# Optimization experiments

Measured on AMD Instinct MI355X. Metric: run time of the kernel, lower is better.

## Reference

```python
import jax, jax.numpy as jnp
import numpy as np

MESSAGE_SIZE = 128
MESSAGE_PASSES = 3
N_BONDS = 7      # Single, Double, Triple, Quadruple, Aromatic, Pi, Universal
N_LAYERS = 8     # 8 bias-free Linear layers, ReLU after the first 7
N_TYPES = 6      # top-4 ranked atoms + atom 0, plus catchall slot (index 5)
ATOM_VALS = [6.0, 7.0, 8.0, 9.0, 16.0, 17.0, 1.0]
TOP_ATOMS = [6.0, 7.0, 8.0, 9.0, 0.0]


def setup_inputs() -> dict:
    key = jax.random.key(0)
    ks = jax.random.split(key, 8)
    B, N, F, D = 128, 128, 75, MESSAGE_SIZE
    g = jax.random.uniform(ks[0], (B, N_BONDS, N, N), dtype=jnp.float32)
    h = jax.random.normal(ks[1], (B, N, F), dtype=jnp.float32)
    # channel 0 carries the atomic number used for GRU routing
    atom_ids = jax.random.randint(ks[2], (B, N), 0, len(ATOM_VALS))
    h = h.at[:, :, 0].set(jnp.asarray(ATOM_VALS, jnp.float32)[atom_ids])
    s = 1.0 / np.sqrt(D)
    msg_W = jax.random.normal(ks[3], (N_BONDS, N_LAYERS, D, D), jnp.float32) * s
    gru_Wih = jax.random.normal(ks[4], (2, N_TYPES, 3 * D, D), jnp.float32) * s  # [regular/universal, type, 3H, H]
    gru_Whh = jax.random.normal(ks[5], (2, N_TYPES, 3 * D, D), jnp.float32) * s
    gru_bih = jax.random.normal(ks[6], (2, N_TYPES, 3 * D), jnp.float32) * s
    gru_bhh = jax.random.normal(ks[7], (2, N_TYPES, 3 * D), jnp.float32) * s
    return dict(g=g, h=h, msg_W=msg_W, gru_Wih=gru_Wih, gru_Whh=gru_Whh,
                gru_bih=gru_bih, gru_bhh=gru_bhh)


def _gru_grouped(x, hx, tid, Wih, Whh, bih, bhh):
    """torch.nn.GRUCell(input=x, hx=hx) with per-node parameter group tid in [0,T).
    Wih/Whh: [T, 3H, H], bih/bhh: [T, 3H]."""
    gx = jnp.einsum('nd,tgd->ntg', x, Wih)   # [n, T, 3H]
    gh = jnp.einsum('nd,tgd->ntg', hx, Whh)
    gx = jnp.take_along_axis(gx, tid[:, None, None], axis=1)[:, 0] + bih[tid]
    gh = jnp.take_along_axis(gh, tid[:, None, None], axis=1)[:, 0] + bhh[tid]
    xr, xz, xn = jnp.split(gx, 3, axis=-1)
    hr, hz, hn = jnp.split(gh, 3, axis=-1)
    r = jax.nn.sigmoid(xr + hr)
    z = jax.nn.sigmoid(xz + hz)
    n = jnp.tanh(xn + r * hn)
    return (1.0 - z) * n + z * hx


def reference(g, h, msg_W, gru_Wih, gru_Whh, gru_bih, gru_bhh):
    B, N, F = h.shape
    D = msg_W.shape[-1]
    h_t = jnp.concatenate([h, jnp.zeros((B, N, D - F), h.dtype)], axis=2)  # [B,N,D]
    atoms = h[:, :, 0].reshape(-1)
    tid = jnp.full(atoms.shape, N_TYPES - 1, jnp.int32)  # default catchall
    for i, a in enumerate(TOP_ATOMS):
        tid = jnp.where(atoms == jnp.float32(a), jnp.int32(i), tid)
    for _ in range(MESSAGE_PASSES):
        # per-bond-type 8-layer bias-free MLP, vectorized over the 7 bond types
        xb = jnp.broadcast_to(h_t[None], (N_BONDS, B, N, D))
        for l in range(N_LAYERS):
            xb = jnp.einsum('kbnd,ked->kbne', xb, msg_W[:, l])
            if l < N_LAYERS - 1:
                xb = jax.nn.relu(xb)
        # bmm aggregation per bond type: m_k = g[:,k] @ xb_k
        m_all = jnp.einsum('bknm,kbmd->kbnd', g, xb)
        m_non = m_all[:N_BONDS - 1].sum(0).reshape(-1, D)
        m_uni = m_all[N_BONDS - 1].reshape(-1, D)
        h_flat = h_t.reshape(-1, D)
        out = _gru_grouped(h_flat, m_non, tid, gru_Wih[0], gru_Whh[0], gru_bih[0], gru_bhh[0])
        out_u = _gru_grouped(h_flat, m_uni, tid, gru_Wih[1], gru_Whh[1], gru_bih[1], gru_bhh[1])
        h_t = (out + out_u).reshape(B, N, D)
    return h_t
```

## Files before the change

### kernel.cpp

```cpp
#include <hip/hip_runtime.h>
#include <math.h>

#define NBOND 7
#define NLAY 8
#define NTYPE 6
#define NNODES 16384
#define PX 136

typedef _Float16 half8 __attribute__((ext_vector_type(8)));
typedef _Float16 half4 __attribute__((ext_vector_type(4)));
typedef float floatx16 __attribute__((ext_vector_type(16)));

__device__ __forceinline__ float sig_(float x) { return 1.0f / (1.0f + __expf(-x)); }
__device__ __forceinline__ int drow_(int reg, int hi) { return (reg & 3) + 8 * (reg >> 2) + 4 * hi; }

__device__ __forceinline__ _Float16 hi_(float v) { return (_Float16)v; }
__device__ __forceinline__ _Float16 lo_(float v) { return (_Float16)(v - (float)(_Float16)v); }

__global__ void setup_kernel(const float* __restrict__ h, float* __restrict__ hT,
                             int* __restrict__ counts, int* __restrict__ bucket)
{
    int gid = blockIdx.x * 256 + threadIdx.x;
    int node = gid >> 7, d = gid & 127;
    hT[gid] = (d < 75) ? h[node * 75 + d] : 0.0f;
    if (gid < NNODES) {
        float a = h[gid * 75];
        int tt = 5;
        if      (a == 6.0f) tt = 0;
        else if (a == 7.0f) tt = 1;
        else if (a == 8.0f) tt = 2;
        else if (a == 9.0f) tt = 3;
        else if (a == 0.0f) tt = 4;
        int slot = atomicAdd(&counts[tt], 1);
        bucket[tt * NNODES + slot] = gid;
    }
}

__global__ void pack_msg_kernel(const float* __restrict__ msgW, _Float16* __restrict__ Wp)
{
    int idx = blockIdx.x * 256 + threadIdx.x;
    if (idx >= NBOND * NLAY * 16 * 128) return;
    int e  = idx & 127;
    int c  = (idx >> 7) & 15;
    int kl = idx >> 11;
    const float* src = msgW + ((size_t)kl * 128 + e) * 128 + c * 8;
    float4 u = *(const float4*)src;
    float4 v = *(const float4*)(src + 4);
    float av[8] = {u.x, u.y, u.z, u.w, v.x, v.y, v.z, v.w};
    half8 hh, ll;
    #pragma unroll
    for (int j = 0; j < 8; ++j) { hh[j] = hi_(av[j]); ll[j] = lo_(av[j]); }
    _Float16* dst = Wp + ((size_t)kl * 16 + c) * 2048;
    *(half8*)(dst + e * 8)        = hh;
    *(half8*)(dst + 1024 + e * 8) = ll;
}

__global__ void pack_gru_kernel(const float* __restrict__ Wih, const float* __restrict__ Whh,
                                _Float16* __restrict__ Wp)
{
    int idx = blockIdx.x * 256 + threadIdx.x;
    if (idx >= 2 * NTYPE * 2 * 16 * 384) return;
    int col = idx % 384;
    int c   = (idx / 384) & 15;
    int vm  = idx / 6144;
    int mat = vm & 1;
    int vt  = vm >> 1;
    const float* src = (mat ? Whh : Wih) + ((size_t)vt * 384 + col) * 128 + c * 8;
    float4 u = *(const float4*)src;
    float4 v = *(const float4*)(src + 4);
    float av[8] = {u.x, u.y, u.z, u.w, v.x, v.y, v.z, v.w};
    half8 hh, ll;
    #pragma unroll
    for (int j = 0; j < 8; ++j) { hh[j] = hi_(av[j]); ll[j] = lo_(av[j]); }
    _Float16* dst = Wp + (size_t)vm * 98304 + (size_t)c * 6144;
    *(half8*)(dst + col * 8)        = hh;
    *(half8*)(dst + 3072 + col * 8) = ll;
}

__global__ __launch_bounds__(256) void mlp_agg_mfma(
    const float* __restrict__ hin, const _Float16* __restrict__ Wp,
    const float* __restrict__ gmat, float* __restrict__ m_non, float* __restrict__ m_uni)
{
    __shared__ _Float16 Xhi[128 * PX];
    __shared__ _Float16 Xlo[128 * PX];

    const int t = threadIdx.x;
    const int kb = blockIdx.x, b = blockIdx.y;
    const int wave = t >> 6, lane = t & 63, lo = lane & 31, hi = lane >> 5;
    const int row = wave * 32 + lo;

    for (int q = t; q < 128 * 32; q += 256) {
        int r = q >> 5, c4 = q & 31;
        float4 v = *(const float4*)(hin + ((size_t)(b * 128 + r)) * 128 + c4 * 4);
        half4 hh, ll;
        hh[0] = hi_(v.x); ll[0] = lo_(v.x);
        hh[1] = hi_(v.y); ll[1] = lo_(v.y);
        hh[2] = hi_(v.z); ll[2] = lo_(v.z);
        hh[3] = hi_(v.w); ll[3] = lo_(v.w);
        *(half4*)(Xhi + r * PX + c4 * 4) = hh;
        *(half4*)(Xlo + r * PX + c4 * 4) = ll;
    }
    __syncthreads();

    floatx16 acc[4];

    #pragma unroll 1
    for (int l = 0; l < NLAY; ++l) {
        #pragma unroll
        for (int ct = 0; ct < 4; ++ct) acc[ct] = (floatx16)0.0f;
        const _Float16* wb = Wp + ((size_t)(kb * NLAY + l) * 16) * 2048;

        #pragma unroll 2
        for (int kk = 0; kk < 8; ++kk) {
            half8 a_h = *(const half8*)(Xhi + row * PX + kk * 16 + hi * 8);
            half8 a_l = *(const half8*)(Xlo + row * PX + kk * 16 + hi * 8);
            const _Float16* bp = wb + (size_t)(kk * 2 + hi) * 2048;
            #pragma unroll
            for (int ct = 0; ct < 4; ++ct) {
                half8 b_h = *(const half8*)(bp + (ct * 32 + lo) * 8);
                half8 b_l = *(const half8*)(bp + 1024 + (ct * 32 + lo) * 8);
                acc[ct] = __builtin_amdgcn_mfma_f32_32x32x16_f16(a_h, b_h, acc[ct], 0, 0, 0);
                acc[ct] = __builtin_amdgcn_mfma_f32_32x32x16_f16(a_h, b_l, acc[ct], 0, 0, 0);
                acc[ct] = __builtin_amdgcn_mfma_f32_32x32x16_f16(a_l, b_h, acc[ct], 0, 0, 0);
            }
        }

        if (l < NLAY - 1) {
            #pragma unroll
            for (int ct = 0; ct < 4; ++ct)
                #pragma unroll
                for (int reg = 0; reg < 16; ++reg) {
                    int n = wave * 32 + drow_(reg, hi);
                    float vv = fmaxf(acc[ct][reg], 0.0f);
                    Xhi[n * PX + ct * 32 + lo] = hi_(vv);
                    Xlo[n * PX + ct * 32 + lo] = lo_(vv);
                }
        } else {
            __syncthreads();
            #pragma unroll
            for (int ct = 0; ct < 4; ++ct)
                #pragma unroll
                for (int s = 0; s < 4; ++s) {
                    int e = ct * 32 + lo, m0 = wave * 32 + 8 * s + 4 * hi;
                    half4 hh, ll;
                    #pragma unroll
                    for (int j = 0; j < 4; ++j) {
                        float vv = acc[ct][4 * s + j];
                        hh[j] = hi_(vv); ll[j] = lo_(vv);
                    }
                    *(half4*)(Xhi + e * PX + m0) = hh;
                    *(half4*)(Xlo + e * PX + m0) = ll;
                }
            __syncthreads();
        }
    }

    #pragma unroll
    for (int ct = 0; ct < 4; ++ct) acc[ct] = (floatx16)0.0f;
    const float* grow = gmat + (size_t)(b * NBOND + kb) * 16384;

    #pragma unroll 2
    for (int kk = 0; kk < 8; ++kk) {
        const float* gp = grow + (size_t)row * 128 + kk * 16 + hi * 8;
        float4 u = *(const float4*)gp, v2 = *(const float4*)(gp + 4);
        float av[8] = {u.x, u.y, u.z, u.w, v2.x, v2.y, v2.z, v2.w};
        half8 a_h, a_l;
        #pragma unroll
        for (int j = 0; j < 8; ++j) { a_h[j] = hi_(av[j]); a_l[j] = lo_(av[j]); }
        #pragma unroll
        for (int ct = 0; ct < 4; ++ct) {
            half8 b_h = *(const half8*)(Xhi + (ct * 32 + lo) * PX + kk * 16 + hi * 8);
            half8 b_l = *(const half8*)(Xlo + (ct * 32 + lo) * PX + kk * 16 + hi * 8);
            acc[ct] = __builtin_amdgcn_mfma_f32_32x32x16_f16(a_h, b_h, acc[ct], 0, 0, 0);
            acc[ct] = __builtin_amdgcn_mfma_f32_32x32x16_f16(a_h, b_l, acc[ct], 0, 0, 0);
            acc[ct] = __builtin_amdgcn_mfma_f32_32x32x16_f16(a_l, b_h, acc[ct], 0, 0, 0);
        }
    }

    if (kb == NBOND - 1) {
        #pragma unroll
        for (int ct = 0; ct < 4; ++ct)
            #pragma unroll
            for (int reg = 0; reg < 16; ++reg) {
                int n = wave * 32 + drow_(reg, hi);
                m_uni[((size_t)(b * 128 + n)) * 128 + ct * 32 + lo] = acc[ct][reg];
            }
    } else {
        #pragma unroll
        for (int ct = 0; ct < 4; ++ct)
            #pragma unroll
            for (int reg = 0; reg < 16; ++reg) {
                int n = wave * 32 + drow_(reg, hi);
                atomicAdd(m_non + ((size_t)(b * 128 + n)) * 128 + ct * 32 + lo, acc[ct][reg]);
            }
    }
}

__global__ __launch_bounds__(256, 3) void gru_mfma(
    const float* __restrict__ hin, float* __restrict__ hout,
    const float* __restrict__ m_non, const float* __restrict__ m_uni,
    const int* __restrict__ counts, const int* __restrict__ bucket,
    const _Float16* __restrict__ Wp, const float* __restrict__ bihp, const float* __restrict__ bhhp)
{
    __shared__ _Float16 Xh[32 * PX], Xl[32 * PX], Mh[32 * PX], Ml[32 * PX];
    __shared__ int bl[32];

    const int t = threadIdx.x, tt = blockIdx.y;
    const int v = blockIdx.z >> 1, rtile = blockIdx.z & 1;
    const int cnt  = counts[tt];
    const int base = blockIdx.x * 64 + rtile * 32;
    if (base >= cnt) return;
    const int nn = min(32, cnt - base);
    if (t < 32) bl[t] = (t < nn) ? bucket[tt * NNODES + base + t] : -1;
    __syncthreads();

    const float* msrc = v ? m_uni : m_non;

    for (int q = t; q < 32 * 32; q += 256) {
        int r = q >> 5, c4 = q & 31;
        float4 xv = make_float4(0.f, 0.f, 0.f, 0.f);
        float4 mv = make_float4(0.f, 0.f, 0.f, 0.f);
        int node = bl[r];
        if (node >= 0) {
            xv = *(const float4*)(hin  + (size_t)node * 128 + c4 * 4);
            mv = *(const float4*)(msrc + (size_t)node * 128 + c4 * 4);
        }
        half4 hh, ll;
        hh[0] = hi_(xv.x); ll[0] = lo_(xv.x);
        hh[1] = hi_(xv.y); ll[1] = lo_(xv.y);
        hh[2] = hi_(xv.z); ll[2] = lo_(xv.z);
        hh[3] = hi_(xv.w); ll[3] = lo_(xv.w);
        *(half4*)(Xh + r * PX + c4 * 4) = hh;
        *(half4*)(Xl + r * PX + c4 * 4) = ll;
        hh[0] = hi_(mv.x); ll[0] = lo_(mv.x);
        hh[1] = hi_(mv.y); ll[1] = lo_(mv.y);
        hh[2] = hi_(mv.z); ll[2] = lo_(mv.z);
        hh[3] = hi_(mv.w); ll[3] = lo_(mv.w);
        *(half4*)(Mh + r * PX + c4 * 4) = hh;
        *(half4*)(Ml + r * PX + c4 * 4) = ll;
    }
    __syncthreads();

    const int wave = t >> 6, lane = t & 63, lo = lane & 31, hi = lane >> 5;
    const int d = wave * 32 + lo;
    const int vt = v * NTYPE + tt;
    const _Float16* pih = Wp + (size_t)(vt * 2 + 0) * 98304;
    const _Float16* phh = Wp + (size_t)(vt * 2 + 1) * 98304;

    floatx16 ar = (floatx16)0.0f, az = (floatx16)0.0f;
    floatx16 ax = (floatx16)0.0f, ah = (floatx16)0.0f;

    #pragma unroll 2
    for (int kk = 0; kk < 8; ++kk) {
        int koff = kk * 16 + hi * 8;
        half8 xh = *(const half8*)(Xh + lo * PX + koff);
        half8 xl = *(const half8*)(Xl + lo * PX + koff);
        half8 mh = *(const half8*)(Mh + lo * PX + koff);
        half8 ml = *(const half8*)(Ml + lo * PX + koff);
        const _Float16* ci = pih + (size_t)(kk * 2 + hi) * 6144;
        const _Float16* ch = phh + (size_t)(kk * 2 + hi) * 6144;
        half8 birh = *(const half8*)(ci + (0   + d) * 8);
        half8 birl = *(const half8*)(ci + 3072 + (0   + d) * 8);
        half8 bizh = *(const half8*)(ci + (128 + d) * 8);
        half8 bizl = *(const half8*)(ci + 3072 + (128 + d) * 8);
        half8 binh = *(const half8*)(ci + (256 + d) * 8);
        half8 binl = *(const half8*)(ci + 3072 + (256 + d) * 8);
        half8 bhrh = *(const half8*)(ch + (0   + d) * 8);
        half8 bhrl = *(const half8*)(ch + 3072 + (0   + d) * 8);
        half8 bhzh = *(const half8*)(ch + (128 + d) * 8);
        half8 bhzl = *(const half8*)(ch + 3072 + (128 + d) * 8);
        half8 bhnh = *(const half8*)(ch + (256 + d) * 8);
        half8 bhnl = *(const half8*)(ch + 3072 + (256 + d) * 8);

        ar = __builtin_amdgcn_mfma_f32_32x32x16_f16(xh, birh, ar, 0, 0, 0);
        ar = __builtin_amdgcn_mfma_f32_32x32x16_f16(xh, birl, ar, 0, 0, 0);
        ar = __builtin_amdgcn_mfma_f32_32x32x16_f16(xl, birh, ar, 0, 0, 0);
        ar = __builtin_amdgcn_mfma_f32_32x32x16_f16(mh, bhrh, ar, 0, 0, 0);
        ar = __builtin_amdgcn_mfma_f32_32x32x16_f16(mh, bhrl, ar, 0, 0, 0);
        ar = __builtin_amdgcn_mfma_f32_32x32x16_f16(ml, bhrh, ar, 0, 0, 0);

        az = __builtin_amdgcn_mfma_f32_32x32x16_f16(xh, bizh, az, 0, 0, 0);
        az = __builtin_amdgcn_mfma_f32_32x32x16_f16(xh, bizl, az, 0, 0, 0);
        az = __builtin_amdgcn_mfma_f32_32x32x16_f16(xl, bizh, az, 0, 0, 0);
        az = __builtin_amdgcn_mfma_f32_32x32x16_f16(mh, bhzh, az, 0, 0, 0);
        az = __builtin_amdgcn_mfma_f32_32x32x16_f16(mh, bhzl, az, 0, 0, 0);
        az = __builtin_amdgcn_mfma_f32_32x32x16_f16(ml, bhzh, az, 0, 0, 0);

        ax = __builtin_amdgcn_mfma_f32_32x32x16_f16(xh, binh, ax, 0, 0, 0);
        ax = __builtin_amdgcn_mfma_f32_32x32x16_f16(xh, binl, ax, 0, 0, 0);
        ax = __builtin_amdgcn_mfma_f32_32x32x16_f16(xl, binh, ax, 0, 0, 0);
        ah = __builtin_amdgcn_mfma_f32_32x32x16_f16(mh, bhnh, ah, 0, 0, 0);
        ah = __builtin_amdgcn_mfma_f32_32x32x16_f16(mh, bhnl, ah, 0, 0, 0);
        ah = __builtin_amdgcn_mfma_f32_32x32x16_f16(ml, bhnh, ah, 0, 0, 0);
    }

    const float* bi = bihp + (size_t)vt * 384;
    const float* bh = bhhp + (size_t)vt * 384;
    float b_r  = bi[d] + bh[d];
    float b_z  = bi[128 + d] + bh[128 + d];
    float b_in = bi[256 + d];
    float b_hn = bh[256 + d];
    #pragma unroll
    for (int reg = 0; reg < 16; ++reg) {
        int n = drow_(reg, hi);
        int node = bl[n];
        if (node < 0) continue;
        float r  = sig_(ar[reg] + b_r);
        float z  = sig_(az[reg] + b_z);
        float nv = tanhf(ax[reg] + b_in + r * (ah[reg] + b_hn));
        float mv = msrc[(size_t)node * 128 + d];
        atomicAdd(hout + (size_t)node * 128 + d, (1.0f - z) * nv + z * mv);
    }
}

extern "C" void kernel_launch(void* const* d_in, const int* in_sizes, int n_in,
                              void* d_out, int out_size, void* d_ws, size_t ws_size,
                              hipStream_t stream) {
    const float* g    = (const float*)d_in[0];
    const float* h    = (const float*)d_in[1];
    const float* msgW = (const float*)d_in[2];
    const float* Wih  = (const float*)d_in[3];
    const float* Whh  = (const float*)d_in[4];
    const float* bih  = (const float*)d_in[5];
    const float* bhh  = (const float*)d_in[6];
    float* h1 = (float*)d_out;

    char* ws = (char*)d_ws;
    float* m_non = (float*)ws;
    float* m_uni = m_non + (size_t)NNODES * 128;
    int* counts  = (int*)(ws + 2 * (size_t)NNODES * 128 * 4);
    int* bucket  = counts + 8;
    _Float16* WpM = (_Float16*)(bucket + NTYPE * NNODES);
    _Float16* WpG = WpM + (size_t)NBOND * NLAY * 16 * 2048;
    float* h0 = (float*)(WpG + (size_t)2 * NTYPE * 2 * 98304);

    (void)hipMemsetAsync(counts, 0, 8 * sizeof(int), stream);
    setup_kernel<<<NNODES * 128 / 256, 256, 0, stream>>>(h, h0, counts, bucket);
    pack_msg_kernel<<<(NBOND * NLAY * 16 * 128 + 255) / 256, 256, 0, stream>>>(msgW, WpM);
    pack_gru_kernel<<<(2 * NTYPE * 2 * 16 * 384 + 255) / 256, 256, 0, stream>>>(Wih, Whh, WpG);

    const float* hin_p[3]  = {h0, h1, h0};
    float*       hout_p[3] = {h1, h0, h1};
    for (int pass = 0; pass < 3; ++pass) {
        (void)hipMemsetAsync(m_non, 0, (size_t)NNODES * 128 * 4, stream);
        (void)hipMemsetAsync(hout_p[pass], 0, (size_t)NNODES * 128 * 4, stream);
        mlp_agg_mfma<<<dim3(NBOND, 128), 256, 0, stream>>>(hin_p[pass], WpM, g, m_non, m_uni);
        gru_mfma<<<dim3(NNODES / 64, NTYPE, 4), 256, 0, stream>>>(hin_p[pass], hout_p[pass],
                                                                  m_non, m_uni, counts, bucket,
                                                                  WpG, bih, bhh);
    }
}
```

Baseline: 908.2 us.

## Software-pipeline weight loads and prefetch adjacency rows into registers

Double-buffers the per-k-step weight fragments in registers, so global loads for the next k-slice (and the next layer's first slice) are issued before the current MFMAs. During the last MLP layer it also prefetches the whole adjacency row block for the aggregation GEMM into registers. It fully unrolls the k loops and sets launch bounds to request 2 blocks per SM. The extra live registers (the 64-float greg array plus the double buffers) risk spills under the occupancy hint.

New measurement: 904.8 us. No clear change (-0.4%).

```diff
diff --git a/kernel.cpp b/kernel.cpp
--- a/kernel.cpp
+++ b/kernel.cpp
@@ -77,7 +77,7 @@
     *(half8*)(dst + 3072 + col * 8) = ll;
 }
 
-__global__ __launch_bounds__(256) void mlp_agg_mfma(
+__global__ __launch_bounds__(256, 2) void mlp_agg_mfma(
     const float* __restrict__ hin, const _Float16* __restrict__ Wp,
     const float* __restrict__ gmat, float* __restrict__ m_non, float* __restrict__ m_uni)
 {
@@ -103,66 +103,119 @@
     __syncthreads();
 
     floatx16 acc[4];
+    half8 bcur_h[4], bcur_l[4];
+
+    {
+        const _Float16* bp = Wp + ((size_t)(kb * NLAY) * 16) * 2048 + (size_t)hi * 2048;
+        #pragma unroll
+        for (int ct = 0; ct < 4; ++ct) {
+            bcur_h[ct] = *(const half8*)(bp + (ct * 32 + lo) * 8);
+            bcur_l[ct] = *(const half8*)(bp + 1024 + (ct * 32 + lo) * 8);
+        }
+    }
 
     #pragma unroll 1
-    for (int l = 0; l < NLAY; ++l) {
+    for (int l = 0; l < NLAY - 1; ++l) {
         #pragma unroll
         for (int ct = 0; ct < 4; ++ct) acc[ct] = (floatx16)0.0f;
         const _Float16* wb = Wp + ((size_t)(kb * NLAY + l) * 16) * 2048;
 
-        #pragma unroll 2
+        #pragma unroll
         for (int kk = 0; kk < 8; ++kk) {
+            half8 bn_h[4], bn_l[4];
+            const _Float16* bp = (kk < 7) ? (wb + (size_t)((kk + 1) * 2 + hi) * 2048)
+                                          : (wb + (size_t)(16 * 2048) + (size_t)hi * 2048);
+            #pragma unroll
+            for (int ct = 0; ct < 4; ++ct) {
+                bn_h[ct] = *(const half8*)(bp + (ct * 32 + lo) * 8);
+                bn_l[ct] = *(const half8*)(bp + 1024 + (ct * 32 + lo) * 8);
+            }
             half8 a_h = *(const half8*)(Xhi + row * PX + kk * 16 + hi * 8);
             half8 a_l = *(const half8*)(Xlo + row * PX + kk * 16 + hi * 8);
-            const _Float16* bp = wb + (size_t)(kk * 2 + hi) * 2048;
             #pragma unroll
             for (int ct = 0; ct < 4; ++ct) {
-                half8 b_h = *(const half8*)(bp + (ct * 32 + lo) * 8);
-                half8 b_l = *(const half8*)(bp + 1024 + (ct * 32 + lo) * 8);
-                acc[ct] = __builtin_amdgcn_mfma_f32_32x32x16_f16(a_h, b_h, acc[ct], 0, 0, 0);
-                acc[ct] = __builtin_amdgcn_mfma_f32_32x32x16_f16(a_h, b_l, acc[ct], 0, 0, 0);
-                acc[ct] = __builtin_amdgcn_mfma_f32_32x32x16_f16(a_l, b_h, acc[ct], 0, 0, 0);
-            }
-        }
-
-        if (l < NLAY - 1) {
-            #pragma unroll
-            for (int ct = 0; ct < 4; ++ct)
+                acc[ct] = __builtin_amdgcn_mfma_f32_32x32x16_f16(a_h, bcur_h[ct], acc[ct], 0, 0, 0);
+                acc[ct] = __builtin_amdgcn_mfma_f32_32x32x16_f16(a_h, bcur_l[ct], acc[ct], 0, 0, 0);
+                acc[ct] = __builtin_amdgcn_mfma_f32_32x32x16_f16(a_l, bcur_h[ct], acc[ct], 0, 0, 0);
+            }
+            #pragma unroll
+            for (int ct = 0; ct < 4; ++ct) { bcur_h[ct] = bn_h[ct]; bcur_l[ct] = bn_l[ct]; }
+        }
+
+        #pragma unroll
+        for (int ct = 0; ct < 4; ++ct)
+            #pragma unroll
+            for (int reg = 0; reg < 16; ++reg) {
+                int n = wave * 32 + drow_(reg, hi);
+                float vv = fmaxf(acc[ct][reg], 0.0f);
+                Xhi[n * PX + ct * 32 + lo] = hi_(vv);
+                Xlo[n * PX + ct * 32 + lo] = lo_(vv);
+            }
+    }
+
+    float4 greg[16];
+    const float* grow = gmat + (size_t)(b * NBOND + kb) * 16384;
+    {
+        #pragma unroll
+        for (int ct = 0; ct < 4; ++ct) acc[ct] = (floatx16)0.0f;
+        const _Float16* wb = Wp + ((size_t)(kb * NLAY + 7) * 16) * 2048;
+
+        #pragma unroll
+        for (int kk = 0; kk < 8; ++kk) {
+            half8 bn_h[4], bn_l[4];
+            if (kk < 7) {
+                const _Float16* bp = wb + (size_t)((kk + 1) * 2 + hi) * 2048;
                 #pragma unroll
-                for (int reg = 0; reg < 16; ++reg) {
-                    int n = wave * 32 + drow_(reg, hi);
-                    float vv = fmaxf(acc[ct][reg], 0.0f);
-                    Xhi[n * PX + ct * 32 + lo] = hi_(vv);
-                    Xlo[n * PX + ct * 32 + lo] = lo_(vv);
+                for (int ct = 0; ct < 4; ++ct) {
+                    bn_h[ct] = *(const half8*)(bp + (ct * 32 + lo) * 8);
+                    bn_l[ct] = *(const half8*)(bp + 1024 + (ct * 32 + lo) * 8);
                 }
-        } else {
-            __syncthreads();
-            #pragma unroll
-            for (int ct = 0; ct < 4; ++ct)
+            } else {
                 #pragma unroll
-                for (int s = 0; s < 4; ++s) {
-                    int e = ct * 32 + lo, m0 = wave * 32 + 8 * s + 4 * hi;
-                    half4 hh, ll;
-                    #pragma unroll
-                    for (int j = 0; j < 4; ++j) {
-                        float vv = acc[ct][4 * s + j];
-                        hh[j] = hi_(vv); ll[j] = lo_(vv);
-                    }
-                    *(half4*)(Xhi + e * PX + m0) = hh;
-                    *(half4*)(Xlo + e * PX + m0) = ll;
+                for (int k2 = 0; k2 < 8; ++k2) {
+                    const float* gp = grow + (size_t)row * 128 + k2 * 16 + hi * 8;
+                    greg[k2 * 2]     = *(const float4*)gp;
+                    greg[k2 * 2 + 1] = *(const float4*)(gp + 4);
                 }
-            __syncthreads();
-        }
-    }
+            }
+            half8 a_h = *(const half8*)(Xhi + row * PX + kk * 16 + hi * 8);
+            half8 a_l = *(const half8*)(Xlo + row * PX + kk * 16 + hi * 8);
+            #pragma unroll
+            for (int ct = 0; ct < 4; ++ct) {
+                acc[ct] = __builtin_amdgcn_mfma_f32_32x32x16_f16(a_h, bcur_h[ct], acc[ct], 0, 0, 0);
+                acc[ct] = __builtin_amdgcn_mfma_f32_32x32x16_f16(a_h, bcur_l[ct], acc[ct], 0, 0, 0);
+                acc[ct] = __builtin_amdgcn_mfma_f32_32x32x16_f16(a_l, bcur_h[ct], acc[ct], 0, 0, 0);
+            }
+            if (kk < 7) {
+                #pragma unroll
+                for (int ct = 0; ct < 4; ++ct) { bcur_h[ct] = bn_h[ct]; bcur_l[ct] = bn_l[ct]; }
+            }
+        }
+    }
+
+    __syncthreads();
+    #pragma unroll
+    for (int ct = 0; ct < 4; ++ct)
+        #pragma unroll
+        for (int s = 0; s < 4; ++s) {
+            int e = ct * 32 + lo, m0 = wave * 32 + 8 * s + 4 * hi;
+            half4 hh, ll;
+            #pragma unroll
+            for (int j = 0; j < 4; ++j) {
+                float vv = acc[ct][4 * s + j];
+                hh[j] = hi_(vv); ll[j] = lo_(vv);
+            }
+            *(half4*)(Xhi + e * PX + m0) = hh;
+            *(half4*)(Xlo + e * PX + m0) = ll;
+        }
+    __syncthreads();
 
     #pragma unroll
     for (int ct = 0; ct < 4; ++ct) acc[ct] = (floatx16)0.0f;
-    const float* grow = gmat + (size_t)(b * NBOND + kb) * 16384;
-
-    #pragma unroll 2
+
+    #pragma unroll
     for (int kk = 0; kk < 8; ++kk) {
-        const float* gp = grow + (size_t)row * 128 + kk * 16 + hi * 8;
-        float4 u = *(const float4*)gp, v2 = *(const float4*)(gp + 4);
+        float4 u = greg[kk * 2], v2 = greg[kk * 2 + 1];
         float av[8] = {u.x, u.y, u.z, u.w, v2.x, v2.y, v2.z, v2.w};
         half8 a_h, a_l;
         #pragma unroll
```

## Remap MLP waves to column tiles; fuse GRU variants and update hidden state in place

Applied to the files above, without the earlier changes.

In the MLP kernel, each wave now owns a 32-column slice of the output across all 128 rows instead of a 32-row slice across all columns. Each weight fragment is then loaded from global memory once per k-step and reused across four row tiles, at the cost of more LDS reads of the activations and an extra block barrier per layer. The GRU kernel now processes both the regular and the universal parameter sets in one block and updates the hidden state in place. This removes the atomicAdd output, the per-pass memset of the output buffer and the ping-pong hidden buffer. The trade-off is fewer GRU blocks, each doing serialized work for the two variants.

Result: faster. 802.0 us (-11.7%).

```diff
diff --git a/kernel.cpp b/kernel.cpp
--- a/kernel.cpp
+++ b/kernel.cpp
@@ -88,6 +88,7 @@
     const int kb = blockIdx.x, b = blockIdx.y;
     const int wave = t >> 6, lane = t & 63, lo = lane & 31, hi = lane >> 5;
     const int row = wave * 32 + lo;
+    const int wcol = wave * 32 + lo;
 
     for (int q = t; q < 128 * 32; q += 256) {
         int r = q >> 5, c4 = q & 31;
@@ -107,52 +108,52 @@
     #pragma unroll 1
     for (int l = 0; l < NLAY; ++l) {
         #pragma unroll
-        for (int ct = 0; ct < 4; ++ct) acc[ct] = (floatx16)0.0f;
+        for (int rt = 0; rt < 4; ++rt) acc[rt] = (floatx16)0.0f;
         const _Float16* wb = Wp + ((size_t)(kb * NLAY + l) * 16) * 2048;
 
-        #pragma unroll 2
+        #pragma unroll
         for (int kk = 0; kk < 8; ++kk) {
-            half8 a_h = *(const half8*)(Xhi + row * PX + kk * 16 + hi * 8);
-            half8 a_l = *(const half8*)(Xlo + row * PX + kk * 16 + hi * 8);
             const _Float16* bp = wb + (size_t)(kk * 2 + hi) * 2048;
-            #pragma unroll
-            for (int ct = 0; ct < 4; ++ct) {
-                half8 b_h = *(const half8*)(bp + (ct * 32 + lo) * 8);
-                half8 b_l = *(const half8*)(bp + 1024 + (ct * 32 + lo) * 8);
-                acc[ct] = __builtin_amdgcn_mfma_f32_32x32x16_f16(a_h, b_h, acc[ct], 0, 0, 0);
-                acc[ct] = __builtin_amdgcn_mfma_f32_32x32x16_f16(a_h, b_l, acc[ct], 0, 0, 0);
-                acc[ct] = __builtin_amdgcn_mfma_f32_32x32x16_f16(a_l, b_h, acc[ct], 0, 0, 0);
+            half8 b_h = *(const half8*)(bp + wcol * 8);
+            half8 b_l = *(const half8*)(bp + 1024 + wcol * 8);
+            #pragma unroll
+            for (int rt = 0; rt < 4; ++rt) {
+                half8 a_h = *(const half8*)(Xhi + (rt * 32 + lo) * PX + kk * 16 + hi * 8);
+                half8 a_l = *(const half8*)(Xlo + (rt * 32 + lo) * PX + kk * 16 + hi * 8);
+                acc[rt] = __builtin_amdgcn_mfma_f32_32x32x16_f16(a_h, b_h, acc[rt], 0, 0, 0);
+                acc[rt] = __builtin_amdgcn_mfma_f32_32x32x16_f16(a_h, b_l, acc[rt], 0, 0, 0);
+                acc[rt] = __builtin_amdgcn_mfma_f32_32x32x16_f16(a_l, b_h, acc[rt], 0, 0, 0);
             }
         }
+        __syncthreads();
 
         if (l < NLAY - 1) {
             #pragma unroll
-            for (int ct = 0; ct < 4; ++ct)
+            for (int rt = 0; rt < 4; ++rt)
                 #pragma unroll
                 for (int reg = 0; reg < 16; ++reg) {
-                    int n = wave * 32 + drow_(reg, hi);
-                    float vv = fmaxf(acc[ct][reg], 0.0f);
-                    Xhi[n * PX + ct * 32 + lo] = hi_(vv);
-                    Xlo[n * PX + ct * 32 + lo] = lo_(vv);
+                    int n = rt * 32 + drow_(reg, hi);
+                    float vv = fmaxf(acc[rt][reg], 0.0f);
+                    Xhi[n * PX + wcol] = hi_(vv);
+                    Xlo[n * PX + wcol] = lo_(vv);
                 }
         } else {
-            __syncthreads();
-            #pragma unroll
-            for (int ct = 0; ct < 4; ++ct)
+            #pragma unroll
+            for (int rt = 0; rt < 4; ++rt)
                 #pragma unroll
                 for (int s = 0; s < 4; ++s) {
-                    int e = ct * 32 + lo, m0 = wave * 32 + 8 * s + 4 * hi;
+                    int m0 = rt * 32 + 8 * s + 4 * hi;
                     half4 hh, ll;
                     #pragma unroll
                     for (int j = 0; j < 4; ++j) {
-                        float vv = acc[ct][4 * s + j];
+                        float vv = acc[rt][4 * s + j];
                         hh[j] = hi_(vv); ll[j] = lo_(vv);
                     }
-                    *(half4*)(Xhi + e * PX + m0) = hh;
-                    *(half4*)(Xlo + e * PX + m0) = ll;
+                    *(half4*)(Xhi + wcol * PX + m0) = hh;
+                    *(half4*)(Xlo + wcol * PX + m0) = ll;
                 }
-            __syncthreads();
-        }
+        }
+        __syncthreads();
     }
 
     #pragma unroll
@@ -197,7 +198,7 @@
 }
 
 __global__ __launch_bounds__(256, 3) void gru_mfma(
-    const float* __restrict__ hin, float* __restrict__ hout,
+    float* __restrict__ hT,
     const float* __restrict__ m_non, const float* __restrict__ m_uni,
     const int* __restrict__ counts, const int* __restrict__ bucket,
     const _Float16* __restrict__ Wp, const float* __restrict__ bihp, const float* __restrict__ bhhp)
@@ -205,8 +206,7 @@
     __shared__ _Float16 Xh[32 * PX], Xl[32 * PX], Mh[32 * PX], Ml[32 * PX];
     __shared__ int bl[32];
 
-    const int t = threadIdx.x, tt = blockIdx.y;
-    const int v = blockIdx.z >> 1, rtile = blockIdx.z & 1;
+    const int t = threadIdx.x, tt = blockIdx.y, rtile = blockIdx.z;
     const int cnt  = counts[tt];
     const int base = blockIdx.x * 64 + rtile * 32;
     if (base >= cnt) return;
@@ -214,17 +214,11 @@
     if (t < 32) bl[t] = (t < nn) ? bucket[tt * NNODES + base + t] : -1;
     __syncthreads();
 
-    const float* msrc = v ? m_uni : m_non;
-
     for (int q = t; q < 32 * 32; q += 256) {
         int r = q >> 5, c4 = q & 31;
         float4 xv = make_float4(0.f, 0.f, 0.f, 0.f);
-        float4 mv = make_float4(0.f, 0.f, 0.f, 0.f);
         int node = bl[r];
-        if (node >= 0) {
-            xv = *(const float4*)(hin  + (size_t)node * 128 + c4 * 4);
-            mv = *(const float4*)(msrc + (size_t)node * 128 + c4 * 4);
-        }
+        if (node >= 0) xv = *(const float4*)(hT + (size_t)node * 128 + c4 * 4);
         half4 hh, ll;
         hh[0] = hi_(xv.x); ll[0] = lo_(xv.x);
         hh[1] = hi_(xv.y); ll[1] = lo_(xv.y);
@@ -232,84 +226,100 @@
         hh[3] = hi_(xv.w); ll[3] = lo_(xv.w);
         *(half4*)(Xh + r * PX + c4 * 4) = hh;
         *(half4*)(Xl + r * PX + c4 * 4) = ll;
-        hh[0] = hi_(mv.x); ll[0] = lo_(mv.x);
-        hh[1] = hi_(mv.y); ll[1] = lo_(mv.y);
-        hh[2] = hi_(mv.z); ll[2] = lo_(mv.z);
-        hh[3] = hi_(mv.w); ll[3] = lo_(mv.w);
-        *(half4*)(Mh + r * PX + c4 * 4) = hh;
-        *(half4*)(Ml + r * PX + c4 * 4) = ll;
-    }
-    __syncthreads();
+    }
 
     const int wave = t >> 6, lane = t & 63, lo = lane & 31, hi = lane >> 5;
     const int d = wave * 32 + lo;
-    const int vt = v * NTYPE + tt;
-    const _Float16* pih = Wp + (size_t)(vt * 2 + 0) * 98304;
-    const _Float16* phh = Wp + (size_t)(vt * 2 + 1) * 98304;
-
-    floatx16 ar = (floatx16)0.0f, az = (floatx16)0.0f;
-    floatx16 ax = (floatx16)0.0f, ah = (floatx16)0.0f;
-
-    #pragma unroll 2
-    for (int kk = 0; kk < 8; ++kk) {
-        int koff = kk * 16 + hi * 8;
-        half8 xh = *(const half8*)(Xh + lo * PX + koff);
-        half8 xl = *(const half8*)(Xl + lo * PX + koff);
-        half8 mh = *(const half8*)(Mh + lo * PX + koff);
-        half8 ml = *(const half8*)(Ml + lo * PX + koff);
-        const _Float16* ci = pih + (size_t)(kk * 2 + hi) * 6144;
-        const _Float16* ch = phh + (size_t)(kk * 2 + hi) * 6144;
-        half8 birh = *(const half8*)(ci + (0   + d) * 8);
-        half8 birl = *(const half8*)(ci + 3072 + (0   + d) * 8);
-        half8 bizh = *(const half8*)(ci + (128 + d) * 8);
-        half8 bizl = *(const half8*)(ci + 3072 + (128 + d) * 8);
-        half8 binh = *(const half8*)(ci + (256 + d) * 8);
-        half8 binl = *(const half8*)(ci + 3072 + (256 + d) * 8);
-        half8 bhrh = *(const half8*)(ch + (0   + d) * 8);
-        half8 bhrl = *(const half8*)(ch + 3072 + (0   + d) * 8);
-        half8 bhzh = *(const half8*)(ch + (128 + d) * 8);
-        half8 bhzl = *(const half8*)(ch + 3072 + (128 + d) * 8);
-        half8 bhnh = *(const half8*)(ch + (256 + d) * 8);
-        half8 bhnl = *(const half8*)(ch + 3072 + (256 + d) * 8);
-
-        ar = __builtin_amdgcn_mfma_f32_32x32x16_f16(xh, birh, ar, 0, 0, 0);
-        ar = __builtin_amdgcn_mfma_f32_32x32x16_f16(xh, birl, ar, 0, 0, 0);
-        ar = __builtin_amdgcn_mfma_f32_32x32x16_f16(xl, birh, ar, 0, 0, 0);
-        ar = __builtin_amdgcn_mfma_f32_32x32x16_f16(mh, bhrh, ar, 0, 0, 0);
-        ar = __builtin_amdgcn_mfma_f32_32x32x16_f16(mh, bhrl, ar, 0, 0, 0);
-        ar = __builtin_amdgcn_mfma_f32_32x32x16_f16(ml, bhrh, ar, 0, 0, 0);
-
-        az = __builtin_amdgcn_mfma_f32_32x32x16_f16(xh, bizh, az, 0, 0, 0);
-        az = __builtin_amdgcn_mfma_f32_32x32x16_f16(xh, bizl, az, 0, 0, 0);
-        az = __builtin_amdgcn_mfma_f32_32x32x16_f16(xl, bizh, az, 0, 0, 0);
-        az = __builtin_amdgcn_mfma_f32_32x32x16_f16(mh, bhzh, az, 0, 0, 0);
-        az = __builtin_amdgcn_mfma_f32_32x32x16_f16(mh, bhzl, az, 0, 0, 0);
-        az = __builtin_amdgcn_mfma_f32_32x32x16_f16(ml, bhzh, az, 0, 0, 0);
-
-        ax = __builtin_amdgcn_mfma_f32_32x32x16_f16(xh, binh, ax, 0, 0, 0);
-        ax = __builtin_amdgcn_mfma_f32_32x32x16_f16(xh, binl, ax, 0, 0, 0);
-        ax = __builtin_amdgcn_mfma_f32_32x32x16_f16(xl, binh, ax, 0, 0, 0);
-        ah = __builtin_amdgcn_mfma_f32_32x32x16_f16(mh, bhnh, ah, 0, 0, 0);
-        ah = __builtin_amdgcn_mfma_f32_32x32x16_f16(mh, bhnl, ah, 0, 0, 0);
-        ah = __builtin_amdgcn_mfma_f32_32x32x16_f16(ml, bhnh, ah, 0, 0, 0);
-    }
-
-    const float* bi = bihp + (size_t)vt * 384;
-    const float* bh = bhhp + (size_t)vt * 384;
-    float b_r  = bi[d] + bh[d];
-    float b_z  = bi[128 + d] + bh[128 + d];
-    float b_in = bi[256 + d];
-    float b_hn = bh[256 + d];
-    #pragma unroll
-    for (int reg = 0; reg < 16; ++reg) {
-        int n = drow_(reg, hi);
-        int node = bl[n];
-        if (node < 0) continue;
-        float r  = sig_(ar[reg] + b_r);
-        float z  = sig_(az[reg] + b_z);
-        float nv = tanhf(ax[reg] + b_in + r * (ah[reg] + b_hn));
-        float mv = msrc[(size_t)node * 128 + d];
-        atomicAdd(hout + (size_t)node * 128 + d, (1.0f - z) * nv + z * mv);
+
+    #pragma unroll 1
+    for (int v = 0; v < 2; ++v) {
+        const float* msrc = v ? m_uni : m_non;
+        __syncthreads();
+        for (int q = t; q < 32 * 32; q += 256) {
+            int r = q >> 5, c4 = q & 31;
+            float4 mv = make_float4(0.f, 0.f, 0.f, 0.f);
+            int node = bl[r];
+            if (node >= 0) mv = *(const float4*)(msrc + (size_t)node * 128 + c4 * 4);
+            half4 hh, ll;
+            hh[0] = hi_(mv.x); ll[0] = lo_(mv.x);
+            hh[1] = hi_(mv.y); ll[1] = lo_(mv.y);
+            hh[2] = hi_(mv.z); ll[2] = lo_(mv.z);
+            hh[3] = hi_(mv.w); ll[3] = lo_(mv.w);
+            *(half4*)(Mh + r * PX + c4 * 4) = hh;
+            *(half4*)(Ml + r * PX + c4 * 4) = ll;
+        }
+        __syncthreads();
+
+        const int vt = v * NTYPE + tt;
+        const _Float16* pih = Wp + (size_t)(vt * 2 + 0) * 98304;
+        const _Float16* phh = Wp + (size_t)(vt * 2 + 1) * 98304;
+
+        floatx16 ar = (floatx16)0.0f, az = (floatx16)0.0f;
+        floatx16 ax = (floatx16)0.0f, ah = (floatx16)0.0f;
+
+        #pragma unroll 2
+        for (int kk = 0; kk < 8; ++kk) {
+            int koff = kk * 16 + hi * 8;
+            half8 xh = *(const half8*)(Xh + lo * PX + koff);
+            half8 xl = *(const half8*)(Xl + lo * PX + koff);
+            half8 mh = *(const half8*)(Mh + lo * PX + koff);
+            half8 ml = *(const half8*)(Ml + lo * PX + koff);
+            const _Float16* ci = pih + (size_t)(kk * 2 + hi) * 6144;
+            const _Float16* ch = phh + (size_t)(kk * 2 + hi) * 6144;
+            half8 birh = *(const half8*)(ci + (0   + d) * 8);
+            half8 birl = *(const half8*)(ci + 3072 + (0   + d) * 8);
+            half8 bizh = *(const half8*)(ci + (128 + d) * 8);
+            half8 bizl = *(const half8*)(ci + 3072 + (128 + d) * 8);
+            half8 binh = *(const half8*)(ci + (256 + d) * 8);
+            half8 binl = *(const half8*)(ci + 3072 + (256 + d) * 8);
+            half8 bhrh = *(const half8*)(ch + (0   + d) * 8);
+            half8 bhrl = *(const half8*)(ch + 3072 + (0   + d) * 8);
+            half8 bhzh = *(const half8*)(ch + (128 + d) * 8);
+            half8 bhzl = *(const half8*)(ch + 3072 + (128 + d) * 8);
+            half8 bhnh = *(const half8*)(ch + (256 + d) * 8);
+            half8 bhnl = *(const half8*)(ch + 3072 + (256 + d) * 8);
+
+            ar = __builtin_amdgcn_mfma_f32_32x32x16_f16(xh, birh, ar, 0, 0, 0);
+            ar = __builtin_amdgcn_mfma_f32_32x32x16_f16(xh, birl, ar, 0, 0, 0);
+            ar = __builtin_amdgcn_mfma_f32_32x32x16_f16(xl, birh, ar, 0, 0, 0);
+            ar = __builtin_amdgcn_mfma_f32_32x32x16_f16(mh, bhrh, ar, 0, 0, 0);
+            ar = __builtin_amdgcn_mfma_f32_32x32x16_f16(mh, bhrl, ar, 0, 0, 0);
+            ar = __builtin_amdgcn_mfma_f32_32x32x16_f16(ml, bhrh, ar, 0, 0, 0);
+
+            az = __builtin_amdgcn_mfma_f32_32x32x16_f16(xh, bizh, az, 0, 0, 0);
+            az = __builtin_amdgcn_mfma_f32_32x32x16_f16(xh, bizl, az, 0, 0, 0);
+            az = __builtin_amdgcn_mfma_f32_32x32x16_f16(xl, bizh, az, 0, 0, 0);
+            az = __builtin_amdgcn_mfma_f32_32x32x16_f16(mh, bhzh, az, 0, 0, 0);
+            az = __builtin_amdgcn_mfma_f32_32x32x16_f16(mh, bhzl, az, 0, 0, 0);
+            az = __builtin_amdgcn_mfma_f32_32x32x16_f16(ml, bhzh, az, 0, 0, 0);
+
+            ax = __builtin_amdgcn_mfma_f32_32x32x16_f16(xh, binh, ax, 0, 0, 0);
+            ax = __builtin_amdgcn_mfma_f32_32x32x16_f16(xh, binl, ax, 0, 0, 0);
+            ax = __builtin_amdgcn_mfma_f32_32x32x16_f16(xl, binh, ax, 0, 0, 0);
+            ah = __builtin_amdgcn_mfma_f32_32x32x16_f16(mh, bhnh, ah, 0, 0, 0);
+            ah = __builtin_amdgcn_mfma_f32_32x32x16_f16(mh, bhnl, ah, 0, 0, 0);
+            ah = __builtin_amdgcn_mfma_f32_32x32x16_f16(ml, bhnh, ah, 0, 0, 0);
+        }
+
+        const float* bi = bihp + (size_t)vt * 384;
+        const float* bh = bhhp + (size_t)vt * 384;
+        float b_r  = bi[d] + bh[d];
+        float b_z  = bi[128 + d] + bh[128 + d];
+        float b_in = bi[256 + d];
+        float b_hn = bh[256 + d];
+        #pragma unroll
+        for (int reg = 0; reg < 16; ++reg) {
+            int n = drow_(reg, hi);
+            int node = bl[n];
+            if (node < 0) continue;
+            float r  = sig_(ar[reg] + b_r);
+            float z  = sig_(az[reg] + b_z);
+            float nv = tanhf(ax[reg] + b_in + r * (ah[reg] + b_hn));
+            float mv = msrc[(size_t)node * 128 + d];
+            float val = (1.0f - z) * nv + z * mv;
+            if (v == 0) hT[(size_t)node * 128 + d] = val;
+            else        hT[(size_t)node * 128 + d] += val;
+        }
     }
 }
 
@@ -323,7 +333,7 @@
     const float* Whh  = (const float*)d_in[4];
     const float* bih  = (const float*)d_in[5];
     const float* bhh  = (const float*)d_in[6];
-    float* h1 = (float*)d_out;
+    float* hT = (float*)d_out;
 
     char* ws = (char*)d_ws;
     float* m_non = (float*)ws;
@@ -332,21 +342,16 @@
     int* bucket  = counts + 8;
     _Float16* WpM = (_Float16*)(bucket + NTYPE * NNODES);
     _Float16* WpG = WpM + (size_t)NBOND * NLAY * 16 * 2048;
-    float* h0 = (float*)(WpG + (size_t)2 * NTYPE * 2 * 98304);
 
     (void)hipMemsetAsync(counts, 0, 8 * sizeof(int), stream);
-    setup_kernel<<<NNODES * 128 / 256, 256, 0, stream>>>(h, h0, counts, bucket);
+    setup_kernel<<<NNODES * 128 / 256, 256, 0, stream>>>(h, hT, counts, bucket);
     pack_msg_kernel<<<(NBOND * NLAY * 16 * 128 + 255) / 256, 256, 0, stream>>>(msgW, WpM);
     pack_gru_kernel<<<(2 * NTYPE * 2 * 16 * 384 + 255) / 256, 256, 0, stream>>>(Wih, Whh, WpG);
 
-    const float* hin_p[3]  = {h0, h1, h0};
-    float*       hout_p[3] = {h1, h0, h1};
     for (int pass = 0; pass < 3; ++pass) {
         (void)hipMemsetAsync(m_non, 0, (size_t)NNODES * 128 * 4, stream);
-        (void)hipMemsetAsync(hout_p[pass], 0, (size_t)NNODES * 128 * 4, stream);
-        mlp_agg_mfma<<<dim3(NBOND, 128), 256, 0, stream>>>(hin_p[pass], WpM, g, m_non, m_uni);
-        gru_mfma<<<dim3(NNODES / 64, NTYPE, 4), 256, 0, stream>>>(hin_p[pass], hout_p[pass],
-                                                                  m_non, m_uni, counts, bucket,
+        mlp_agg_mfma<<<dim3(NBOND, 128), 256, 0, stream>>>(hT, WpM, g, m_non, m_uni);
+        gru_mfma<<<dim3(NNODES / 64, NTYPE, 2), 256, 0, stream>>>(hT, m_non, m_uni, counts, bucket,
                                                                   WpG, bih, bhh);
     }
 }
```
